# Kernel tuning notes

Measured on AMD Instinct MI355X. Metric: run time of the kernel, lower is better.

Reference implementation:

```python
import jax, jax.numpy as jnp
import numpy as np

N_NODES = 20000
N_EDGES = 320000
T = 4
H = 128


def setup_inputs() -> dict:
    key = jax.random.key(0)
    k = jax.random.split(key, 8)
    nf = jax.random.normal(k[0], (N_NODES, T, H), dtype=jnp.float32)
    input_events = jax.random.randint(k[1], (N_NODES, T), 0, 2, dtype=jnp.int32)
    src = jax.random.randint(k[2], (N_EDGES,), 0, N_NODES, dtype=jnp.int32)
    dst = jax.random.randint(k[3], (N_EDGES,), 0, N_NODES, dtype=jnp.int32)
    # attention params (GAT-style additive attention, decomposed a = [a_src; a_dst])
    a_src = jax.random.normal(k[4], (H,), dtype=jnp.float32) / np.sqrt(H)
    a_dst = jax.random.normal(k[5], (H,), dtype=jnp.float32) / np.sqrt(H)
    # node model: Linear(2*h_dim -> h_dim) + ReLU (mpnn built with 2*h_dim input)
    W = jax.random.normal(k[6], (2 * H, H), dtype=jnp.float32) / np.sqrt(2 * H)
    b = jnp.zeros((H,), dtype=jnp.float32)
    return {"nf": nf, "input_events": input_events, "src": src, "dst": dst,
            "a_src": a_src, "a_dst": a_dst, "W": W, "b": b}


def reference(nf, input_events, src, dst, a_src, a_dst, W, b):
    # Vectorized over all T timesteps at once. An edge participates at timestep t
    # iff input_events[src_node, t] == 1 (this replaces the per-node nonzero loop).
    N = nf.shape[0]
    neg_inf = jnp.asarray(-1e9, nf.dtype)

    # per-node attention projections: [N, T]
    proj_s = jnp.einsum("nth,h->nt", nf, a_src)
    proj_d = jnp.einsum("nth,h->nt", nf, a_dst)

    logits = jax.nn.leaky_relu(proj_s[src] + proj_d[dst], 0.2)   # [E, T]
    active = input_events[src] == 1                               # [E, T]
    logits = jnp.where(active, logits, neg_inf)

    # masked segment softmax over incoming active edges of each dst node
    m = jax.ops.segment_max(logits, dst, num_segments=N)          # [N, T]
    ex = jnp.where(active, jnp.exp(logits - m[dst]), 0.0)         # [E, T]
    den = jax.ops.segment_sum(ex, dst, num_segments=N)            # [N, T]
    alpha = ex / jnp.maximum(den[dst], 1e-9)                      # [E, T]

    # aggregate attention-weighted source features: [N, T, H]
    msgs = alpha[..., None] * nf[src]                             # [E, T, H]
    agg = jax.ops.segment_sum(msgs, dst, num_segments=N)          # [N, T, H]

    # node update on concat([nf, agg]) -> 2*h_dim input, ReLU
    out = jax.nn.relu(jnp.concatenate([nf, agg], axis=-1) @ W + b)
    return out
```

## Files before the change

kernel.cpp:

```cpp
#include <hip/hip_runtime.h>
#include <hip/hip_bf16.h>
#include <math.h>

#define NN 20000
#define NE 320000
#define TT 4
#define HH 128
#define NT4 (NN * TT)
#define CAP 128

typedef __attribute__((ext_vector_type(8))) short short8v;
typedef __attribute__((ext_vector_type(4))) float f32x4;

static __device__ __forceinline__ unsigned short f2bf(float v) {
    union { float f; unsigned u; } x; x.f = v;
    unsigned r = x.u + 0x7fff + ((x.u >> 16) & 1);
    return (unsigned short)(r >> 16);
}
static __device__ __forceinline__ unsigned pack2bf(float a, float b) {
    return (unsigned)f2bf(a) | ((unsigned)f2bf(b) << 16);
}
static __device__ __forceinline__ float bf_lo(unsigned v) { return __uint_as_float(v << 16); }
static __device__ __forceinline__ float bf_hi(unsigned v) { return __uint_as_float(v & 0xffff0000u); }


__global__ __launch_bounds__(256) void fusedA_kernel(
        const float* __restrict__ nf, const int* __restrict__ events,
        const float* __restrict__ a_src, const float* __restrict__ a_dst,
        const float* __restrict__ W,
        float* __restrict__ psm, float* __restrict__ pdv,
        unsigned* __restrict__ nfbt, int* __restrict__ cnt,
        uint4* __restrict__ wp) {
    int blk = blockIdx.x, tid = threadIdx.x;
    if (blk < 2500) {
        int g = tid >> 4, l16 = tid & 15;
        int rowA = blk * 32 + g;
        int rowB = rowA + 16;
        const float4* nf4 = (const float4*)nf;
        float4 va0 = nf4[(size_t)rowA * 32 + l16 * 2];
        float4 va1 = nf4[(size_t)rowA * 32 + l16 * 2 + 1];
        float4 vb0 = nf4[(size_t)rowB * 32 + l16 * 2];
        float4 vb1 = nf4[(size_t)rowB * 32 + l16 * 2 + 1];
        float4 s0 = ((const float4*)a_src)[l16 * 2];
        float4 s1 = ((const float4*)a_src)[l16 * 2 + 1];
        float4 d0 = ((const float4*)a_dst)[l16 * 2];
        float4 d1 = ((const float4*)a_dst)[l16 * 2 + 1];

        float sA = va0.x*s0.x + va0.y*s0.y + va0.z*s0.z + va0.w*s0.w
                 + va1.x*s1.x + va1.y*s1.y + va1.z*s1.z + va1.w*s1.w;
        float dA = va0.x*d0.x + va0.y*d0.y + va0.z*d0.z + va0.w*d0.w
                 + va1.x*d1.x + va1.y*d1.y + va1.z*d1.z + va1.w*d1.w;
        float sB = vb0.x*s0.x + vb0.y*s0.y + vb0.z*s0.z + vb0.w*s0.w
                 + vb1.x*s1.x + vb1.y*s1.y + vb1.z*s1.z + vb1.w*s1.w;
        float dB = vb0.x*d0.x + vb0.y*d0.y + vb0.z*d0.z + vb0.w*d0.w
                 + vb1.x*d1.x + vb1.y*d1.y + vb1.z*d1.z + vb1.w*d1.w;

        int nA = rowA >> 2, tA = rowA & 3;
        int nB = rowB >> 2;
        uint4 qa;
        qa.x = pack2bf(va0.x, va0.y); qa.y = pack2bf(va0.z, va0.w);
        qa.z = pack2bf(va1.x, va1.y); qa.w = pack2bf(va1.z, va1.w);
        ((uint4*)nfbt)[((size_t)tA * NN + nA) * 16 + l16] = qa;
        uint4 qb;
        qb.x = pack2bf(vb0.x, vb0.y); qb.y = pack2bf(vb0.z, vb0.w);
        qb.z = pack2bf(vb1.x, vb1.y); qb.w = pack2bf(vb1.z, vb1.w);
        ((uint4*)nfbt)[((size_t)tA * NN + nB) * 16 + l16] = qb;

        #pragma unroll
        for (int o = 1; o < 16; o <<= 1) {
            sA += __shfl_xor(sA, o); dA += __shfl_xor(dA, o);
            sB += __shfl_xor(sB, o); dB += __shfl_xor(dB, o);
        }
        if (l16 == 0) {
            psm[rowA] = (events[rowA] == 1) ? sA : -1e30f;
            pdv[rowA] = dA;
            psm[rowB] = (events[rowB] == 1) ? sB : -1e30f;
            pdv[rowB] = dB;
        }
    } else if (blk < 2516) {
        int f = (blk - 2500) * 256 + tid;
        int lane  = f & 63;
        int tile  = f >> 6;
        int kstep = tile >> 3, ntile = tile & 7;
        int k0 = kstep * 32 + (lane >> 4) * 8;
        int n  = ntile * 16 + (lane & 15);
        unsigned short h[8];
        #pragma unroll
        for (int j = 0; j < 8; ++j)
            h[j] = f2bf(W[(size_t)(k0 + j) * HH + n]);
        uint4 q;
        q.x = h[0] | ((unsigned)h[1] << 16);
        q.y = h[2] | ((unsigned)h[3] << 16);
        q.z = h[4] | ((unsigned)h[5] << 16);
        q.w = h[6] | ((unsigned)h[7] << 16);
        wp[f] = q;
    } else {
        int idx = (blk - 2516) * 256 + tid;
        #pragma unroll
        for (int k = 0; k < 4; ++k) {
            int j = idx * 4 + k;
            if (j < NN) cnt[j] = 0;
        }
    }
}

__global__ void scatterA_kernel(const int* __restrict__ src, const int* __restrict__ dst,
                                const float* __restrict__ psm, const float* __restrict__ pdv,
                                int* __restrict__ cnt, uint4* __restrict__ sexe, int n) {
    int e = blockIdx.x * blockDim.x + threadIdx.x;
    if (e >= n) return;
    int s = src[e], d = dst[e];
    float4 ps4 = *(const float4*)&psm[s * 4];
    bool any = (ps4.x > -1e29f) | (ps4.y > -1e29f) | (ps4.z > -1e29f) | (ps4.w > -1e29f);
    if (!any) return;
    int pos = atomicAdd(&cnt[d], 1);
    if (pos >= CAP) return;
    float4 pd4 = *(const float4*)&pdv[d * 4];
    float x0 = ps4.x + pd4.x; x0 = (x0 > 0.f) ? x0 : 0.2f * x0;
    float x1 = ps4.y + pd4.y; x1 = (x1 > 0.f) ? x1 : 0.2f * x1;
    float x2 = ps4.z + pd4.z; x2 = (x2 > 0.f) ? x2 : 0.2f * x2;
    float x3 = ps4.w + pd4.w; x3 = (x3 > 0.f) ? x3 : 0.2f * x3;
    float e0 = __expf(x0), e1 = __expf(x1), e2 = __expf(x2), e3 = __expf(x3);
    uint4 q;
    q.x = (unsigned)s;
    q.y = pack2bf(e0, e1);
    q.z = pack2bf(e2, e3);
    q.w = 0;
    sexe[(size_t)d * CAP + pos] = q;
}

__global__ __launch_bounds__(256) void aggA_kernel(
        const unsigned* __restrict__ nfbt,
        const int* __restrict__ cnt,
        const uint4* __restrict__ sexe,
        unsigned* __restrict__ aggb) {
    __shared__ int2 led[4][64];
    int w    = threadIdx.x >> 6;
    int lane = threadIdx.x & 63;
    int t    = blockIdx.x / (NN / 4);
    int d    = (blockIdx.x % (NN / 4)) * 4 + w;
    int cd   = cnt[d]; if (cd > CAP) cd = CAP;
    size_t off = (size_t)d * CAP;
    int half = lane >> 5, sl = lane & 31;
    const unsigned* nft = nfbt + ((size_t)t * NN << 6);

    float a0 = 0.f, a1 = 0.f, a2 = 0.f, a3 = 0.f;
    float den = 0.f;
    for (int base = 0; base < cd; base += 64) {
        int i = base + lane;
        int s = 0; float ex = 0.f;
        if (i < cd) {
            uint4 q = sexe[off + i];
            s = (int)q.x;
            unsigned packed = (t & 2) ? q.z : q.y;
            ex = (t & 1) ? bf_hi(packed) : bf_lo(packed);
        }
        den += ex;
        unsigned long long mask = __ballot(ex > 0.f);
        int nact = __popcll(mask);
        if (ex > 0.f) {
            int pos = __popcll(mask & ((1ull << lane) - 1ull));
            led[w][pos] = make_int2(s, __float_as_int(ex));
        }
        int j = 0;
        for (; j + 8 <= nact; j += 8) {
            #pragma unroll
            for (int u = 0; u < 4; ++u) {
                int2 a = led[w][j + 2 * u + half];
                uint2 v = *(const uint2*)&nft[((size_t)a.x << 6) + sl * 2];
                float e = __int_as_float(a.y);
                a0 += e * bf_lo(v.x); a1 += e * bf_hi(v.x);
                a2 += e * bf_lo(v.y); a3 += e * bf_hi(v.y);
            }
        }
        for (; j < nact; j += 2) {
            int idx = j + half;
            if (idx < nact) {
                int2 a = led[w][idx];
                uint2 v = *(const uint2*)&nft[((size_t)a.x << 6) + sl * 2];
                float e = __int_as_float(a.y);
                a0 += e * bf_lo(v.x); a1 += e * bf_hi(v.x);
                a2 += e * bf_lo(v.y); a3 += e * bf_hi(v.y);
            }
        }
    }
    #pragma unroll
    for (int o = 32; o >= 1; o >>= 1) den += __shfl_xor(den, o);
    a0 += __shfl_xor(a0, 32); a1 += __shfl_xor(a1, 32);
    a2 += __shfl_xor(a2, 32); a3 += __shfl_xor(a3, 32);
    float scale = (den > 0.f) ? (1.f / den) : 0.f;
    if (half == 0) {
        int dt = d * TT + t;
        uint2 o2;
        o2.x = pack2bf(a0 * scale, a1 * scale);
        o2.y = pack2bf(a2 * scale, a3 * scale);
        *(uint2*)&aggb[((size_t)dt << 6) + sl * 2] = o2;
    }
}

__global__ __launch_bounds__(256) void outA_kernel(
        const uint4* __restrict__ nfbt4, const uint4* __restrict__ wp,
        const float* __restrict__ b, const uint4* __restrict__ aggb4,
        float* __restrict__ out) {
    __shared__ uint4 xs[2048];
    int tid = threadIdx.x;
    size_t row0 = (size_t)blockIdx.x * 64;

    #pragma unroll
    for (int i = 0; i < 8; ++i) {
        int c = i * 256 + tid;
        int row = c >> 5, kc = c & 31;
        size_t grow = row0 + row;
        uint4 q;
        if (kc < 16) {
            size_t nidx = ((grow & 3) * NN + (grow >> 2));
            q = nfbt4[nidx * 16 + kc];
        } else {
            q = aggb4[grow * 16 + (kc - 16)];
        }
        xs[(row * 32 + kc) ^ (row & 7)] = q;
    }
    __syncthreads();

    int w = tid >> 6, l = tid & 63;
    f32x4 acc[8];
    #pragma unroll
    for (int nt = 0; nt < 8; ++nt) acc[nt] = (f32x4){0.f, 0.f, 0.f, 0.f};

    int arow = w * 16 + (l & 15);
    const uint4* wplane = wp + l;
    #pragma unroll
    for (int ks = 0; ks < 8; ++ks) {
        int kc = ks * 4 + (l >> 4);
        uint4 av = xs[(arow * 32 + kc) ^ (arow & 7)];
        short8v af = __builtin_bit_cast(short8v, av);
        #pragma unroll
        for (int nt = 0; nt < 8; ++nt) {
            uint4 bv = wplane[(ks * 8 + nt) * 64];
            short8v bf = __builtin_bit_cast(short8v, bv);
            acc[nt] = __builtin_amdgcn_mfma_f32_16x16x32_bf16(bf, af, acc[nt], 0, 0, 0);
        }
    }

    int col = l & 15;
    int oq  = (l >> 4) * 4;
    size_t orow = (row0 + w * 16 + col) * HH;
    #pragma unroll
    for (int nt = 0; nt < 8; ++nt) {
        float4 bv4 = *(const float4*)&b[nt * 16 + oq];
        float4 res;
        res.x = fmaxf(acc[nt][0] + bv4.x, 0.f);
        res.y = fmaxf(acc[nt][1] + bv4.y, 0.f);
        res.z = fmaxf(acc[nt][2] + bv4.z, 0.f);
        res.w = fmaxf(acc[nt][3] + bv4.w, 0.f);
        *(float4*)&out[orow + nt * 16 + oq] = res;
    }
}

__global__ void projB_kernel(const float* __restrict__ nf,
                             const int* __restrict__ events,
                             const float* __restrict__ a_src,
                             const float* __restrict__ a_dst,
                             float* __restrict__ psm, float* __restrict__ pdv,
                             int total) {
    int wid  = (blockIdx.x * blockDim.x + threadIdx.x) >> 6;
    int lane = threadIdx.x & 63;
    if (wid >= total) return;
    float2 v  = ((const float2*)nf)[(size_t)wid * 64 + lane];
    float2 as = ((const float2*)a_src)[lane];
    float2 ad = ((const float2*)a_dst)[lane];
    float s  = v.x * as.x + v.y * as.y;
    float dd = v.x * ad.x + v.y * ad.y;
    #pragma unroll
    for (int o = 32; o >= 1; o >>= 1) {
        s  += __shfl_xor(s, o);
        dd += __shfl_xor(dd, o);
    }
    if (lane == 0) {
        psm[wid] = (events[wid] == 1) ? s : -1e30f;
        pdv[wid] = dd;
    }
}

__global__ void histB_kernel(const int* __restrict__ dst, int* __restrict__ deg, int n) {
    int e = blockIdx.x * blockDim.x + threadIdx.x;
    if (e < n) atomicAdd(&deg[dst[e]], 1);
}

__global__ __launch_bounds__(1024) void scan1_kernel(
        const int* __restrict__ deg, int* __restrict__ offsets,
        int* __restrict__ bsum, int n) {
    __shared__ int wsum[16];
    int tid = threadIdx.x, lane = tid & 63, wid = tid >> 6;
    int i = blockIdx.x * 1024 + tid;
    int v = (i < n) ? deg[i] : 0;
    int inc = v;
    #pragma unroll
    for (int o = 1; o < 64; o <<= 1) {
        int x = __shfl_up(inc, o);
        if (lane >= o) inc += x;
    }
    if (lane == 63) wsum[wid] = inc;
    __syncthreads();
    if (wid == 0 && lane < 16) {
        int t = wsum[lane];
        int w2 = t;
        #pragma unroll
        for (int o = 1; o < 16; o <<= 1) {
            int x = __shfl_up(w2, o);
            if (lane >= o) w2 += x;
        }
        wsum[lane] = w2 - t;
    }
    __syncthreads();
    int incl = wsum[wid] + inc;
    if (i < n) offsets[i + 1] = incl;
    if (tid == 1023) bsum[blockIdx.x] = incl;
}

__global__ __launch_bounds__(1024) void scan2_kernel(
        const int* __restrict__ bsum, int* __restrict__ offsets,
        int* __restrict__ cursor, int n) {
    __shared__ int base_s;
    int tid = threadIdx.x, blk = blockIdx.x;
    if (tid < 64) {
        int s = 0;
        for (int j = tid; j < blk; j += 64) s += bsum[j];
        #pragma unroll
        for (int o = 32; o >= 1; o >>= 1) s += __shfl_xor(s, o);
        if (tid == 0) base_s = s;
    }
    __syncthreads();
    int i = blk * 1024 + tid;
    if (i < n) {
        int v = offsets[i + 1] + base_s;
        offsets[i + 1] = v;
        cursor[i + 1]  = v;
    }
    if (blk == 0 && tid == 0) { offsets[0] = 0; cursor[0] = 0; }
}

__global__ void scatterB_kernel(const int* __restrict__ src, const int* __restrict__ dst,
                                int* __restrict__ cursor, int* __restrict__ ssrc, int n) {
    int e = blockIdx.x * blockDim.x + threadIdx.x;
    if (e < n) {
        int pos = atomicAdd(&cursor[dst[e]], 1);
        ssrc[pos] = src[e];
    }
}

__global__ __launch_bounds__(256) void aggB_kernel(
        const float* __restrict__ nf,
        const float* __restrict__ psm,
        const float* __restrict__ pdv,
        const int* __restrict__ offsets,
        const int* __restrict__ ssrc,
        float* __restrict__ agg) {
    __shared__ int2 led[TT][64];
    int t    = threadIdx.x >> 6;
    int lane = threadIdx.x & 63;
    int d    = blockIdx.x;
    int off = offsets[d], end = offsets[d + 1];
    float pd = pdv[d * TT + t];
    const float2* nf2 = (const float2*)nf;
    size_t tl = (size_t)t * 64 + lane;

    float2 acc = {0.f, 0.f};
    float den = 0.f;
    for (int base = off; base < end; base += 64) {
        int i = base + lane;
        float ex = 0.f; int s = 0;
        if (i < end) {
            s = ssrc[i];
            float p = psm[s * TT + t];
            if (p > -1e29f) {
                float x = p + pd;
                x = (x > 0.f) ? x : 0.2f * x;
                ex = __expf(x);
            }
        }
        den += ex;
        unsigned long long mask = __ballot(ex > 0.f);
        int nact = __popcll(mask);
        if (ex > 0.f) {
            int pos = __popcll(mask & ((1ull << lane) - 1ull));
            led[t][pos] = make_int2(s, __float_as_int(ex));
        }
        int j = 0;
        for (; j + 4 <= nact; j += 4) {
            int2 a0 = led[t][j], a1 = led[t][j + 1], a2 = led[t][j + 2], a3 = led[t][j + 3];
            float2 r0 = nf2[(size_t)a0.x * 256 + tl];
            float2 r1 = nf2[(size_t)a1.x * 256 + tl];
            float2 r2 = nf2[(size_t)a2.x * 256 + tl];
            float2 r3 = nf2[(size_t)a3.x * 256 + tl];
            float e0 = __int_as_float(a0.y), e1 = __int_as_float(a1.y);
            float e2 = __int_as_float(a2.y), e3 = __int_as_float(a3.y);
            acc.x += e0 * r0.x; acc.y += e0 * r0.y;
            acc.x += e1 * r1.x; acc.y += e1 * r1.y;
            acc.x += e2 * r2.x; acc.y += e2 * r2.y;
            acc.x += e3 * r3.x; acc.y += e3 * r3.y;
        }
        for (; j < nact; ++j) {
            int2 a = led[t][j];
            float2 r = nf2[(size_t)a.x * 256 + tl];
            float e = __int_as_float(a.y);
            acc.x += e * r.x; acc.y += e * r.y;
        }
    }
    #pragma unroll
    for (int o = 32; o >= 1; o >>= 1) den += __shfl_xor(den, o);
    float scale = (den > 0.f) ? (1.f / den) : 0.f;
    float2 res; res.x = acc.x * scale; res.y = acc.y * scale;
    ((float2*)agg)[(size_t)d * 256 + tl] = res;
}

__global__ void wpackB_kernel(const float* __restrict__ W, uint4* __restrict__ wp) {
    int f = blockIdx.x * blockDim.x + threadIdx.x;
    if (f >= 8 * 8 * 64) return;
    int lane  = f & 63;
    int tile  = f >> 6;
    int kstep = tile >> 3, ntile = tile & 7;
    int k0 = kstep * 32 + (lane >> 4) * 8;
    int n  = ntile * 16 + (lane & 15);
    unsigned short h[8];
    #pragma unroll
    for (int j = 0; j < 8; ++j)
        h[j] = f2bf(W[(size_t)(k0 + j) * HH + n]);
    uint4 q;
    q.x = h[0] | ((unsigned)h[1] << 16);
    q.y = h[2] | ((unsigned)h[3] << 16);
    q.z = h[4] | ((unsigned)h[5] << 16);
    q.w = h[6] | ((unsigned)h[7] << 16);
    wp[f] = q;
}

__global__ __launch_bounds__(256) void outB_kernel(
        const float* __restrict__ nf, const uint4* __restrict__ wp,
        const float* __restrict__ b, float* __restrict__ out) {
    __shared__ uint4 xs[2048];
    int tid = threadIdx.x;
    size_t row0 = (size_t)blockIdx.x * 64;

    #pragma unroll
    for (int i = 0; i < 8; ++i) {
        int c = i * 256 + tid;
        int row = c >> 5, kc = c & 31;
        const float* srcp = (kc < 16) ? (nf  + (row0 + row) * HH + kc * 8)
                                      : (out + (row0 + row) * HH + (kc - 16) * 8);
        float4 v0 = *reinterpret_cast<const float4*>(srcp);
        float4 v1 = *reinterpret_cast<const float4*>(srcp + 4);
        uint4 q;
        q.x = pack2bf(v0.x, v0.y);
        q.y = pack2bf(v0.z, v0.w);
        q.z = pack2bf(v1.x, v1.y);
        q.w = pack2bf(v1.z, v1.w);
        xs[(row * 32 + kc) ^ (row & 7)] = q;
    }
    __syncthreads();

    int w = tid >> 6, l = tid & 63;
    f32x4 acc[8];
    #pragma unroll
    for (int nt = 0; nt < 8; ++nt) acc[nt] = (f32x4){0.f, 0.f, 0.f, 0.f};

    int arow = w * 16 + (l & 15);
    const uint4* wplane = wp + l;
    #pragma unroll
    for (int ks = 0; ks < 8; ++ks) {
        int kc = ks * 4 + (l >> 4);
        uint4 av = xs[(arow * 32 + kc) ^ (arow & 7)];
        short8v af = __builtin_bit_cast(short8v, av);
        #pragma unroll
        for (int nt = 0; nt < 8; ++nt) {
            uint4 bv = wplane[(ks * 8 + nt) * 64];
            short8v bf = __builtin_bit_cast(short8v, bv);
            acc[nt] = __builtin_amdgcn_mfma_f32_16x16x32_bf16(bf, af, acc[nt], 0, 0, 0);
        }
    }

    int col = l & 15;
    int oq  = (l >> 4) * 4;
    size_t orow = (row0 + w * 16 + col) * HH;
    #pragma unroll
    for (int nt = 0; nt < 8; ++nt) {
        float4 bv4 = *(const float4*)&b[nt * 16 + oq];
        float4 res;
        res.x = fmaxf(acc[nt][0] + bv4.x, 0.f);
        res.y = fmaxf(acc[nt][1] + bv4.y, 0.f);
        res.z = fmaxf(acc[nt][2] + bv4.z, 0.f);
        res.w = fmaxf(acc[nt][3] + bv4.w, 0.f);
        *(float4*)&out[orow + nt * 16 + oq] = res;
    }
}

extern "C" void kernel_launch(void* const* d_in, const int* in_sizes, int n_in,
                              void* d_out, int out_size, void* d_ws, size_t ws_size,
                              hipStream_t stream) {
    const float* nf      = (const float*)d_in[0];
    const int*   events  = (const int*)  d_in[1];
    const int*   src     = (const int*)  d_in[2];
    const int*   dst     = (const int*)  d_in[3];
    const float* a_src   = (const float*)d_in[4];
    const float* a_dst   = (const float*)d_in[5];
    const float* W       = (const float*)d_in[6];
    const float* b       = (const float*)d_in[7];
    float* out = (float*)d_out;

    const int total_nt = NT4;
    char* ws = (char*)d_ws;

    const size_t NEED_A = 41745664;
    if (ws_size >= NEED_A) {
        unsigned* nfbt  = (unsigned*)(ws);
        unsigned* aggb  = (unsigned*)(ws + 20480000);
        float* psm      = (float*)(ws + 40960000);
        float* pdv      = (float*)(ws + 41280000);
        int*   cnt      = (int*)  (ws + 41600000);
        uint4* wpack    = (uint4*)(ws + 41680128);
        uint4* sexe     = (uint4*)d_out;

        fusedA_kernel<<<2536, 256, 0, stream>>>(nf, events, a_src, a_dst, W,
                                                psm, pdv, nfbt, cnt, wpack);
        scatterA_kernel<<<(NE + 255) / 256, 256, 0, stream>>>(src, dst, psm, pdv,
                                                              cnt, sexe, NE);
        aggA_kernel<<<NN, 256, 0, stream>>>(nfbt, cnt, sexe, aggb);
        outA_kernel<<<total_nt / 64, 256, 0, stream>>>((const uint4*)nfbt, wpack, b,
                                                       (const uint4*)aggb, out);
    } else {
        float* psm     = (float*)(ws);
        float* pdv     = (float*)(ws + 1310720);
        int*   offsets = (int*)  (ws + 2621440);
        int*   deg     = (int*)  (ws + 2703360);
        int*   cursor  = (int*)  (ws + 2785280);
        int*   ssrc    = (int*)  (ws + 2867200);
        uint4* wpack   = (uint4*)(ws);
        int*   bsumB   = (int*)  (ws + 4147200);

        const int SCAN_B = (NN + 1023) / 1024;
        hipMemsetAsync(deg, 0, NN * sizeof(int), stream);
        projB_kernel<<<total_nt / 4, 256, 0, stream>>>(nf, events, a_src, a_dst, psm, pdv, total_nt);
        histB_kernel<<<(NE + 255) / 256, 256, 0, stream>>>(dst, deg, NE);
        scan1_kernel<<<SCAN_B, 1024, 0, stream>>>(deg, offsets, bsumB, NN);
        scan2_kernel<<<SCAN_B, 1024, 0, stream>>>(bsumB, offsets, cursor, NN);
        scatterB_kernel<<<(NE + 255) / 256, 256, 0, stream>>>(src, dst, cursor, ssrc, NE);
        aggB_kernel<<<NN, 256, 0, stream>>>(nf, psm, pdv, offsets, ssrc, out);
        wpackB_kernel<<<16, 256, 0, stream>>>(W, wpack);
        outB_kernel<<<total_nt / 64, 256, 0, stream>>>(nf, wpack, b, out);
    }
}
```

Before: 91.67 us.

## Fuse attention aggregation into output GEMM kernel, keeping aggregates in LDS

The separate aggregation and output kernels are merged into one. Each block now aggregates 16 destination nodes directly into the shared-memory A-tile and then runs the MFMA node update. This removes the global round-trip of the bf16 aggregate buffer and one kernel launch. The work mapping also changes: each 16-lane group handles one timestep and loads 8 bf16 per lane, and each wave processes 4 nodes one after another. In exchange the grid is much smaller, per-edge branches can diverge across timestep groups, and the gather latency is serialized inside each wave.

New measurement: 116.0 us. 26.6% more time.

```diff
diff --git a/kernel.cpp b/kernel.cpp
--- a/kernel.cpp
+++ b/kernel.cpp
@@ -129,100 +129,81 @@
     sexe[(size_t)d * CAP + pos] = q;
 }
 
-__global__ __launch_bounds__(256) void aggA_kernel(
-        const unsigned* __restrict__ nfbt,
-        const int* __restrict__ cnt,
-        const uint4* __restrict__ sexe,
-        unsigned* __restrict__ aggb) {
-    __shared__ int2 led[4][64];
-    int w    = threadIdx.x >> 6;
-    int lane = threadIdx.x & 63;
-    int t    = blockIdx.x / (NN / 4);
-    int d    = (blockIdx.x % (NN / 4)) * 4 + w;
-    int cd   = cnt[d]; if (cd > CAP) cd = CAP;
-    size_t off = (size_t)d * CAP;
-    int half = lane >> 5, sl = lane & 31;
-    const unsigned* nft = nfbt + ((size_t)t * NN << 6);
-
-    float a0 = 0.f, a1 = 0.f, a2 = 0.f, a3 = 0.f;
-    float den = 0.f;
-    for (int base = 0; base < cd; base += 64) {
-        int i = base + lane;
-        int s = 0; float ex = 0.f;
-        if (i < cd) {
-            uint4 q = sexe[off + i];
-            s = (int)q.x;
-            unsigned packed = (t & 2) ? q.z : q.y;
-            ex = (t & 1) ? bf_hi(packed) : bf_lo(packed);
-        }
-        den += ex;
-        unsigned long long mask = __ballot(ex > 0.f);
-        int nact = __popcll(mask);
-        if (ex > 0.f) {
-            int pos = __popcll(mask & ((1ull << lane) - 1ull));
-            led[w][pos] = make_int2(s, __float_as_int(ex));
-        }
-        int j = 0;
-        for (; j + 8 <= nact; j += 8) {
-            #pragma unroll
-            for (int u = 0; u < 4; ++u) {
-                int2 a = led[w][j + 2 * u + half];
-                uint2 v = *(const uint2*)&nft[((size_t)a.x << 6) + sl * 2];
-                float e = __int_as_float(a.y);
-                a0 += e * bf_lo(v.x); a1 += e * bf_hi(v.x);
-                a2 += e * bf_lo(v.y); a3 += e * bf_hi(v.y);
+__global__ __launch_bounds__(256) void aggoutA_kernel(
+        const uint4* __restrict__ nfbt4, const int* __restrict__ cnt,
+        const uint4* __restrict__ sexe, const uint4* __restrict__ wp,
+        const float* __restrict__ b, float* __restrict__ out) {
+    __shared__ uint4 xs[2048];
+    __shared__ uint4 led[4][64];
+    int tid = threadIdx.x;
+    int n0 = blockIdx.x * 16;
+    size_t row0 = (size_t)blockIdx.x * 64;
+
+    #pragma unroll
+    for (int i = 0; i < 4; ++i) {
+        int c = i * 256 + tid;
+        int row = c >> 4, kc = c & 15;
+        int n = n0 + (row >> 2), t = row & 3;
+        uint4 q = nfbt4[((size_t)t * NN + n) * 16 + kc];
+        xs[(row * 32 + kc) ^ (row & 7)] = q;
+    }
+
+    int w = tid >> 6, lane = tid & 63;
+    int g = lane >> 4, l16 = lane & 15;
+    const uint4* nft = nfbt4 + (size_t)g * NN * 16;
+    for (int k = 0; k < 4; ++k) {
+        int d = n0 + w * 4 + k;
+        int cd = cnt[d]; if (cd > CAP) cd = CAP;
+        size_t off = (size_t)d * CAP;
+        float a0=0.f,a1=0.f,a2=0.f,a3=0.f,a4=0.f,a5=0.f,a6=0.f,a7=0.f;
+        float den = 0.f;
+        for (int base = 0; base < cd; base += 64) {
+            int i = base + lane;
+            if (i < cd) led[w][lane] = sexe[off + i];
+            int cnt2 = min(64, cd - base);
+            int j = 0;
+            for (; j + 4 <= cnt2; j += 4) {
+                #pragma unroll
+                for (int u = 0; u < 4; ++u) {
+                    uint4 q = led[w][j + u];
+                    unsigned packed = (g & 2) ? q.z : q.y;
+                    float ex = (g & 1) ? bf_hi(packed) : bf_lo(packed);
+                    den += ex;
+                    if (ex > 0.f) {
+                        uint4 v = nft[(size_t)q.x * 16 + l16];
+                        a0 += ex * bf_lo(v.x); a1 += ex * bf_hi(v.x);
+                        a2 += ex * bf_lo(v.y); a3 += ex * bf_hi(v.y);
+                        a4 += ex * bf_lo(v.z); a5 += ex * bf_hi(v.z);
+                        a6 += ex * bf_lo(v.w); a7 += ex * bf_hi(v.w);
+                    }
+                }
             }
-        }
-        for (; j < nact; j += 2) {
-            int idx = j + half;
-            if (idx < nact) {
-                int2 a = led[w][idx];
-                uint2 v = *(const uint2*)&nft[((size_t)a.x << 6) + sl * 2];
-                float e = __int_as_float(a.y);
-                a0 += e * bf_lo(v.x); a1 += e * bf_hi(v.x);
-                a2 += e * bf_lo(v.y); a3 += e * bf_hi(v.y);
+            for (; j < cnt2; ++j) {
+                uint4 q = led[w][j];
+                unsigned packed = (g & 2) ? q.z : q.y;
+                float ex = (g & 1) ? bf_hi(packed) : bf_lo(packed);
+                den += ex;
+                if (ex > 0.f) {
+                    uint4 v = nft[(size_t)q.x * 16 + l16];
+                    a0 += ex * bf_lo(v.x); a1 += ex * bf_hi(v.x);
+                    a2 += ex * bf_lo(v.y); a3 += ex * bf_hi(v.y);
+                    a4 += ex * bf_lo(v.z); a5 += ex * bf_hi(v.z);
+                    a6 += ex * bf_lo(v.w); a7 += ex * bf_hi(v.w);
+                }
             }
         }
-    }
-    #pragma unroll
-    for (int o = 32; o >= 1; o >>= 1) den += __shfl_xor(den, o);
-    a0 += __shfl_xor(a0, 32); a1 += __shfl_xor(a1, 32);
-    a2 += __shfl_xor(a2, 32); a3 += __shfl_xor(a3, 32);
-    float scale = (den > 0.f) ? (1.f / den) : 0.f;
-    if (half == 0) {
-        int dt = d * TT + t;
-        uint2 o2;
-        o2.x = pack2bf(a0 * scale, a1 * scale);
-        o2.y = pack2bf(a2 * scale, a3 * scale);
-        *(uint2*)&aggb[((size_t)dt << 6) + sl * 2] = o2;
-    }
-}
-
-__global__ __launch_bounds__(256) void outA_kernel(
-        const uint4* __restrict__ nfbt4, const uint4* __restrict__ wp,
-        const float* __restrict__ b, const uint4* __restrict__ aggb4,
-        float* __restrict__ out) {
-    __shared__ uint4 xs[2048];
-    int tid = threadIdx.x;
-    size_t row0 = (size_t)blockIdx.x * 64;
-
-    #pragma unroll
-    for (int i = 0; i < 8; ++i) {
-        int c = i * 256 + tid;
-        int row = c >> 5, kc = c & 31;
-        size_t grow = row0 + row;
-        uint4 q;
-        if (kc < 16) {
-            size_t nidx = ((grow & 3) * NN + (grow >> 2));
-            q = nfbt4[nidx * 16 + kc];
-        } else {
-            q = aggb4[grow * 16 + (kc - 16)];
-        }
-        xs[(row * 32 + kc) ^ (row & 7)] = q;
+        float scale = (den > 0.f) ? (1.f / den) : 0.f;
+        int lrow = (w * 4 + k) * 4 + g;
+        uint4 o;
+        o.x = pack2bf(a0 * scale, a1 * scale);
+        o.y = pack2bf(a2 * scale, a3 * scale);
+        o.z = pack2bf(a4 * scale, a5 * scale);
+        o.w = pack2bf(a6 * scale, a7 * scale);
+        xs[(lrow * 32 + 16 + l16) ^ (lrow & 7)] = o;
     }
     __syncthreads();
 
-    int w = tid >> 6, l = tid & 63;
+    int l = lane;
     f32x4 acc[8];
     #pragma unroll
     for (int nt = 0; nt < 8; ++nt) acc[nt] = (f32x4){0.f, 0.f, 0.f, 0.f};
@@ -509,23 +490,21 @@
     const int total_nt = NT4;
     char* ws = (char*)d_ws;
 
-    const size_t NEED_A = 41745664;
+    const size_t NEED_A = 21265664;
     if (ws_size >= NEED_A) {
         unsigned* nfbt  = (unsigned*)(ws);
-        unsigned* aggb  = (unsigned*)(ws + 20480000);
-        float* psm      = (float*)(ws + 40960000);
-        float* pdv      = (float*)(ws + 41280000);
-        int*   cnt      = (int*)  (ws + 41600000);
-        uint4* wpack    = (uint4*)(ws + 41680128);
+        float* psm      = (float*)(ws + 20480000);
+        float* pdv      = (float*)(ws + 20800000);
+        int*   cnt      = (int*)  (ws + 21120000);
+        uint4* wpack    = (uint4*)(ws + 21200128);
         uint4* sexe     = (uint4*)d_out;
 
         fusedA_kernel<<<2536, 256, 0, stream>>>(nf, events, a_src, a_dst, W,
                                                 psm, pdv, nfbt, cnt, wpack);
         scatterA_kernel<<<(NE + 255) / 256, 256, 0, stream>>>(src, dst, psm, pdv,
                                                               cnt, sexe, NE);
-        aggA_kernel<<<NN, 256, 0, stream>>>(nfbt, cnt, sexe, aggb);
-        outA_kernel<<<total_nt / 64, 256, 0, stream>>>((const uint4*)nfbt, wpack, b,
-                                                       (const uint4*)aggb, out);
+        aggoutA_kernel<<<NN / 16, 256, 0, stream>>>((const uint4*)nfbt, cnt, sexe,
+                                                    wpack, b, out);
     } else {
         float* psm     = (float*)(ws);
         float* pdv     = (float*)(ws + 1310720);
```
